# Kernel tuning notes

Measured on AMD Instinct MI355X. Metric: run time of the kernel, lower is better.

The kernel has to match this reference:

```python
import jax, jax.numpy as jnp
import numpy as np

RES = (64, 64)
TEMP = 0.1  # forward default temp

def _mgrid(res):
    # matches torch.meshgrid(linspace(0, r-1, r)...) with default 'ij' indexing
    gs = jnp.meshgrid(*[jnp.arange(r, dtype=jnp.float32) for r in res], indexing='ij')
    return jnp.stack(gs, 0)  # [2, H, W]

def setup_inputs() -> dict:
    key = jax.random.key(0)
    k1, k2 = jax.random.split(key)
    x = jax.random.normal(k1, (8, 32, RES[0], RES[1]), dtype=jnp.float32)
    of = jax.random.normal(k2, (8, 2, RES[0], RES[1]), dtype=jnp.float32)
    return {"x": x, "of": of}

def reference(x, of):
    bs, C = x.shape[0], x.shape[1]
    hw = RES[0] * RES[1]
    gpos = _mgrid(RES).reshape(2, hw)                 # [2, HW] target pixel positions
    opos = gpos[None] + of.reshape(bs, 2, hw)         # [bs, 2, HW] flow-displaced source positions
    # L1 distance: logits[b, i, j] = sum_c |opos[b, c, j] - gpos[c, i]|
    dist = jnp.abs(opos[:, :, None, :] - gpos[None, :, :, None]).sum(axis=1)  # [bs, HW, HW]
    # softmax over target axis i (dim=-2 in torch) -> each source pixel j distributes mass over targets
    locs = jax.nn.softmax(-dist / TEMP, axis=1)       # [bs, HW, HW]
    # out[b, c, i] = sum_j x[b, c, j] * locs[b, i, j]
    out = jnp.einsum('bij,bcj->bci', locs, x.reshape(bs, C, hw))
    return out.reshape(bs, C, RES[0], RES[1])
```

## Files before the change

kernel.cpp:

```cpp
#include <hip/hip_runtime.h>
#include <math.h>

#define HW    4096
#define NC    32
#define NB    8
#define TINV  10.0f
#define RWIN  8
#define WDIM  (8 + 2 * RWIN)
#define RCUT  2.5f


__global__ __launch_bounds__(256) void prep_kernel(
    const float* __restrict__ x, const float* __restrict__ of,
    float4* __restrict__ params, float* __restrict__ xt)
{
    __shared__ float tile[32][257];
    int b  = blockIdx.x >> 4;
    int j0 = (blockIdx.x & 15) << 8;
    int t  = threadIdx.x;
    int j  = j0 + t;

    float oy = (float)(j >> 6) + of[(b * 2 + 0) * HW + j];
    float ox = (float)(j & 63) + of[(b * 2 + 1) * HW + j];

    int cy0 = min(max((int)floorf(oy), 0), 63);
    int cx0 = min(max((int)floorf(ox), 0), 63);
    float Dy = 0.f, Dx = 0.f;
    #pragma unroll
    for (int d = -3; d <= 3; ++d) {
        int iy = cy0 + d, ix = cx0 + d;
        if ((unsigned)iy < 64u) Dy += __expf(-TINV * fabsf(oy - (float)iy));
        if ((unsigned)ix < 64u) Dx += __expf(-TINV * fabsf(ox - (float)ix));
    }
    params[(b << 12) + j] = make_float4(oy, ox, 1.f / Dy, 1.f / Dx);

    #pragma unroll
    for (int c = 0; c < NC; ++c)
        tile[c][t] = x[((b * NC + c) << 12) + j];
    __syncthreads();
    #pragma unroll
    for (int k = 0; k < NC; ++k) {
        int o  = k * 256 + t;
        int jj = o >> 5, c = o & 31;
        xt[((size_t)((b << 12) + j0 + jj)) * NC + c] = tile[c][jj];
    }
}

__global__ __launch_bounds__(256) void gather_kernel(
    const float4* __restrict__ params, const float4* __restrict__ xt4,
    float* __restrict__ out)
{
    __shared__ float  red[4 * 64 * 17];
    __shared__ float4 wp[4][64];
    __shared__ int    sj[4][64];

    const int b    = blockIdx.z;
    const int h    = blockIdx.y;
    const int tile = blockIdx.x;
    const int ty0  = (tile >> 3) << 3;
    const int tx0  = (tile & 7) << 3;

    const int tid  = threadIdx.x;
    const int lane = tid & 63;
    const int wv   = __builtin_amdgcn_readfirstlane(tid >> 6);

    const float iy = (float)(ty0 + (lane >> 3));
    const float ix = (float)(tx0 + (lane & 7));

    float acc[16];
    #pragma unroll
    for (int c = 0; c < 16; ++c) acc[c] = 0.f;

    const float4* pb = params + (b << 12);
    const float4* xb = xt4 + (size_t)(b << 12) * 8 + h * 4;

    const int srow = lane >> 5;
    const int scol = lane & 31;

    for (int r = 0; r < 3; ++r) {
        int ry = wv + srow * 4 + r * 8;
        int jy = ty0 - RWIN + ry;
        int jx = tx0 - RWIN + scol;
        bool valid = ((unsigned)jy < 64u) && ((unsigned)jx < 64u) && (scol < WDIM);
        int j = (jy << 6) + jx;
        float4 p = pb[valid ? j : 0];
        float cy = fminf(fmaxf(p.x, 0.f), 63.f);
        float cx = fminf(fmaxf(p.y, 0.f), 63.f);
        float dyr = fmaxf(fmaxf((float)ty0 - cy, cy - ((float)ty0 + 7.f)), 0.f);
        float dxr = fmaxf(fmaxf((float)tx0 - cx, cx - ((float)tx0 + 7.f)), 0.f);
        bool pred = valid && (dyr + dxr < RCUT);

        unsigned long long m = __ballot(pred);
        int cnt = __popcll(m);
        if (pred) {
            int pos = __builtin_amdgcn_mbcnt_hi((unsigned)(m >> 32),
                      __builtin_amdgcn_mbcnt_lo((unsigned)m, 0u));
            wp[wv][pos] = p;
            sj[wv][pos] = j;
        }

        for (int k = 0; k < cnt; k += 4) {
            int i0 = k;
            int i1 = min(k + 1, cnt - 1);
            int i2 = min(k + 2, cnt - 1);
            int i3 = min(k + 3, cnt - 1);
            float4 p0 = wp[wv][i0], p1 = wp[wv][i1];
            float4 p2 = wp[wv][i2], p3 = wp[wv][i3];
            int j0 = __builtin_amdgcn_readfirstlane(sj[wv][i0]);
            int j1 = __builtin_amdgcn_readfirstlane(sj[wv][i1]);
            int j2 = __builtin_amdgcn_readfirstlane(sj[wv][i2]);
            int j3 = __builtin_amdgcn_readfirstlane(sj[wv][i3]);

            const float4* x0 = xb + j0 * 8;
            const float4* x1 = xb + j1 * 8;
            const float4* x2 = xb + j2 * 8;
            const float4* x3 = xb + j3 * 8;
            float4 A[4], B[4], C[4], D[4];
            #pragma unroll
            for (int u = 0; u < 4; ++u) A[u] = x0[u];
            #pragma unroll
            for (int u = 0; u < 4; ++u) B[u] = x1[u];
            #pragma unroll
            for (int u = 0; u < 4; ++u) C[u] = x2[u];
            #pragma unroll
            for (int u = 0; u < 4; ++u) D[u] = x3[u];

            float g0 = (__expf(-TINV * fabsf(p0.x - iy)) * p0.z)
                     * (__expf(-TINV * fabsf(p0.y - ix)) * p0.w);
            float g1 = (__expf(-TINV * fabsf(p1.x - iy)) * p1.z)
                     * (__expf(-TINV * fabsf(p1.y - ix)) * p1.w);
            float g2 = (__expf(-TINV * fabsf(p2.x - iy)) * p2.z)
                     * (__expf(-TINV * fabsf(p2.y - ix)) * p2.w);
            float g3 = (__expf(-TINV * fabsf(p3.x - iy)) * p3.z)
                     * (__expf(-TINV * fabsf(p3.y - ix)) * p3.w);
            g1 = (k + 1 < cnt) ? g1 : 0.f;
            g2 = (k + 2 < cnt) ? g2 : 0.f;
            g3 = (k + 3 < cnt) ? g3 : 0.f;

            #pragma unroll
            for (int u = 0; u < 4; ++u) {
                acc[4*u+0] = fmaf(g0, A[u].x, acc[4*u+0]);
                acc[4*u+1] = fmaf(g0, A[u].y, acc[4*u+1]);
                acc[4*u+2] = fmaf(g0, A[u].z, acc[4*u+2]);
                acc[4*u+3] = fmaf(g0, A[u].w, acc[4*u+3]);
            }
            #pragma unroll
            for (int u = 0; u < 4; ++u) {
                acc[4*u+0] = fmaf(g1, B[u].x, acc[4*u+0]);
                acc[4*u+1] = fmaf(g1, B[u].y, acc[4*u+1]);
                acc[4*u+2] = fmaf(g1, B[u].z, acc[4*u+2]);
                acc[4*u+3] = fmaf(g1, B[u].w, acc[4*u+3]);
            }
            #pragma unroll
            for (int u = 0; u < 4; ++u) {
                acc[4*u+0] = fmaf(g2, C[u].x, acc[4*u+0]);
                acc[4*u+1] = fmaf(g2, C[u].y, acc[4*u+1]);
                acc[4*u+2] = fmaf(g2, C[u].z, acc[4*u+2]);
                acc[4*u+3] = fmaf(g2, C[u].w, acc[4*u+3]);
            }
            #pragma unroll
            for (int u = 0; u < 4; ++u) {
                acc[4*u+0] = fmaf(g3, D[u].x, acc[4*u+0]);
                acc[4*u+1] = fmaf(g3, D[u].y, acc[4*u+1]);
                acc[4*u+2] = fmaf(g3, D[u].z, acc[4*u+2]);
                acc[4*u+3] = fmaf(g3, D[u].w, acc[4*u+3]);
            }
        }
    }

    float* myred = red + (wv * 64 + lane) * 17;
    #pragma unroll
    for (int c = 0; c < 16; ++c) myred[c] = acc[c];
    __syncthreads();

    int c   = tid >> 4;
    int t16 = tid & 15;
    #pragma unroll
    for (int k = 0; k < 4; ++k) {
        int t = t16 + 16 * k;
        float s = red[(0 * 64 + t) * 17 + c]
                + red[(1 * 64 + t) * 17 + c]
                + red[(2 * 64 + t) * 17 + c]
                + red[(3 * 64 + t) * 17 + c];
        int ch = h * 16 + c;
        out[(((b << 5) + ch) << 12) + (ty0 + (t >> 3)) * 64 + (tx0 + (t & 7))] = s;
    }
}

extern "C" void kernel_launch(void* const* d_in, const int* in_sizes, int n_in,
                              void* d_out, int out_size, void* d_ws, size_t ws_size,
                              hipStream_t stream) {
    const float* x  = (const float*)d_in[0];
    const float* of = (const float*)d_in[1];
    float* out = (float*)d_out;

    float4* params = (float4*)d_ws;
    float*  xt     = (float*)((char*)d_ws + NB * HW * sizeof(float4));

    prep_kernel<<<dim3(NB * 16), dim3(256), 0, stream>>>(x, of, params, xt);
    gather_kernel<<<dim3(64, 2, NB), dim3(256), 0, stream>>>(params, (const float4*)xt, out);
}
```

Baseline: 74.64 us.

## Compact candidate list across rows and software-pipeline gathers with register-held indices

Each wave now runs the candidate selection for all three row passes first, building one compacted list of up to 192 entries in shared memory, then walks it in a single loop. The loop is software-pipelined, so the feature loads for the next pair of candidates are issued before the FMAs for the current pair. Source indices sit in three per-lane registers and are picked out with readlane instead of being read back from shared memory. This removes per-row loop tails and exposes more load latency hiding, at the cost of more registers and a larger shared-memory footprint.

```diff
diff --git a/kernel.cpp b/kernel.cpp
--- a/kernel.cpp
+++ b/kernel.cpp
@@ -6,8 +6,9 @@
 #define NB    8
 #define TINV  10.0f
 #define RWIN  8
-#define WDIM  (8 + 2 * RWIN)
+#define WDIM  24
 #define RCUT  2.5f
+#define LCAP  192
 
 
 __global__ __launch_bounds__(256) void prep_kernel(
@@ -46,13 +47,45 @@
     }
 }
 
+#define FETCH(idx, Xb, Pb) do {                                         \
+    int ic  = min((idx), cm1);                                          \
+    int sel = ic >> 6;                                                  \
+    int jv  = (sel == 0) ? vj0 : ((sel == 1) ? vj1 : vj2);              \
+    int jj  = __builtin_amdgcn_readlane(jv, ic & 63);                   \
+    const float4* xp = xb + jj * 8;                                     \
+    Xb[0] = xp[0]; Xb[1] = xp[1]; Xb[2] = xp[2]; Xb[3] = xp[3];         \
+    Pb = wp[wv][ic];                                                    \
+} while (0)
+
+#define COMPUTE(Xb, Pb, idx) do {                                       \
+    float gy = __expf(-TINV * fabsf(Pb.x - iy)) * Pb.z;                 \
+    float gx = __expf(-TINV * fabsf(Pb.y - ix)) * Pb.w;                 \
+    float g  = ((idx) < cnt) ? gy * gx : 0.f;                           \
+    acc[ 0] = fmaf(g, Xb[0].x, acc[ 0]);                                \
+    acc[ 1] = fmaf(g, Xb[0].y, acc[ 1]);                                \
+    acc[ 2] = fmaf(g, Xb[0].z, acc[ 2]);                                \
+    acc[ 3] = fmaf(g, Xb[0].w, acc[ 3]);                                \
+    acc[ 4] = fmaf(g, Xb[1].x, acc[ 4]);                                \
+    acc[ 5] = fmaf(g, Xb[1].y, acc[ 5]);                                \
+    acc[ 6] = fmaf(g, Xb[1].z, acc[ 6]);                                \
+    acc[ 7] = fmaf(g, Xb[1].w, acc[ 7]);                                \
+    acc[ 8] = fmaf(g, Xb[2].x, acc[ 8]);                                \
+    acc[ 9] = fmaf(g, Xb[2].y, acc[ 9]);                                \
+    acc[10] = fmaf(g, Xb[2].z, acc[10]);                                \
+    acc[11] = fmaf(g, Xb[2].w, acc[11]);                                \
+    acc[12] = fmaf(g, Xb[3].x, acc[12]);                                \
+    acc[13] = fmaf(g, Xb[3].y, acc[13]);                                \
+    acc[14] = fmaf(g, Xb[3].z, acc[14]);                                \
+    acc[15] = fmaf(g, Xb[3].w, acc[15]);                                \
+} while (0)
+
 __global__ __launch_bounds__(256) void gather_kernel(
     const float4* __restrict__ params, const float4* __restrict__ xt4,
     float* __restrict__ out)
 {
     __shared__ float  red[4 * 64 * 17];
-    __shared__ float4 wp[4][64];
-    __shared__ int    sj[4][64];
+    __shared__ float4 wp[4][LCAP];
+    __shared__ int    sj[4][LCAP];
 
     const int b    = blockIdx.z;
     const int h    = blockIdx.y;
@@ -77,6 +110,8 @@
     const int srow = lane >> 5;
     const int scol = lane & 31;
 
+    int cnt = 0;
+    #pragma unroll
     for (int r = 0; r < 3; ++r) {
         int ry = wv + srow * 4 + r * 8;
         int jy = ty0 - RWIN + ry;
@@ -91,80 +126,37 @@
         bool pred = valid && (dyr + dxr < RCUT);
 
         unsigned long long m = __ballot(pred);
-        int cnt = __popcll(m);
         if (pred) {
-            int pos = __builtin_amdgcn_mbcnt_hi((unsigned)(m >> 32),
-                      __builtin_amdgcn_mbcnt_lo((unsigned)m, 0u));
+            int pos = cnt + __builtin_amdgcn_mbcnt_hi((unsigned)(m >> 32),
+                            __builtin_amdgcn_mbcnt_lo((unsigned)m, 0u));
             wp[wv][pos] = p;
             sj[wv][pos] = j;
         }
+        cnt += __popcll(m);
+    }
 
-        for (int k = 0; k < cnt; k += 4) {
-            int i0 = k;
-            int i1 = min(k + 1, cnt - 1);
-            int i2 = min(k + 2, cnt - 1);
-            int i3 = min(k + 3, cnt - 1);
-            float4 p0 = wp[wv][i0], p1 = wp[wv][i1];
-            float4 p2 = wp[wv][i2], p3 = wp[wv][i3];
-            int j0 = __builtin_amdgcn_readfirstlane(sj[wv][i0]);
-            int j1 = __builtin_amdgcn_readfirstlane(sj[wv][i1]);
-            int j2 = __builtin_amdgcn_readfirstlane(sj[wv][i2]);
-            int j3 = __builtin_amdgcn_readfirstlane(sj[wv][i3]);
+    int vj0 = sj[wv][lane];
+    int vj1 = sj[wv][64 + lane];
+    int vj2 = sj[wv][128 + lane];
 
-            const float4* x0 = xb + j0 * 8;
-            const float4* x1 = xb + j1 * 8;
-            const float4* x2 = xb + j2 * 8;
-            const float4* x3 = xb + j3 * 8;
-            float4 A[4], B[4], C[4], D[4];
-            #pragma unroll
-            for (int u = 0; u < 4; ++u) A[u] = x0[u];
-            #pragma unroll
-            for (int u = 0; u < 4; ++u) B[u] = x1[u];
-            #pragma unroll
-            for (int u = 0; u < 4; ++u) C[u] = x2[u];
-            #pragma unroll
-            for (int u = 0; u < 4; ++u) D[u] = x3[u];
-
-            float g0 = (__expf(-TINV * fabsf(p0.x - iy)) * p0.z)
-                     * (__expf(-TINV * fabsf(p0.y - ix)) * p0.w);
-            float g1 = (__expf(-TINV * fabsf(p1.x - iy)) * p1.z)
-                     * (__expf(-TINV * fabsf(p1.y - ix)) * p1.w);
-            float g2 = (__expf(-TINV * fabsf(p2.x - iy)) * p2.z)
-                     * (__expf(-TINV * fabsf(p2.y - ix)) * p2.w);
-            float g3 = (__expf(-TINV * fabsf(p3.x - iy)) * p3.z)
-                     * (__expf(-TINV * fabsf(p3.y - ix)) * p3.w);
-            g1 = (k + 1 < cnt) ? g1 : 0.f;
-            g2 = (k + 2 < cnt) ? g2 : 0.f;
-            g3 = (k + 3 < cnt) ? g3 : 0.f;
-
-            #pragma unroll
-            for (int u = 0; u < 4; ++u) {
-                acc[4*u+0] = fmaf(g0, A[u].x, acc[4*u+0]);
-                acc[4*u+1] = fmaf(g0, A[u].y, acc[4*u+1]);
-                acc[4*u+2] = fmaf(g0, A[u].z, acc[4*u+2]);
-                acc[4*u+3] = fmaf(g0, A[u].w, acc[4*u+3]);
+    if (cnt > 0) {
+        const int cm1  = cnt - 1;
+        const int cnt4 = (cnt + 3) & ~3;
+        float4 X0[4], X1[4], X2[4], X3[4];
+        float4 P0, P1, P2, P3;
+        FETCH(0, X0, P0);
+        FETCH(1, X1, P1);
+        for (int k = 0; k < cnt4; k += 4) {
+            FETCH(k + 2, X2, P2);
+            FETCH(k + 3, X3, P3);
+            COMPUTE(X0, P0, k + 0);
+            COMPUTE(X1, P1, k + 1);
+            if (k + 4 < cnt4) {
+                FETCH(k + 4, X0, P0);
+                FETCH(k + 5, X1, P1);
             }
-            #pragma unroll
-            for (int u = 0; u < 4; ++u) {
-                acc[4*u+0] = fmaf(g1, B[u].x, acc[4*u+0]);
-                acc[4*u+1] = fmaf(g1, B[u].y, acc[4*u+1]);
-                acc[4*u+2] = fmaf(g1, B[u].z, acc[4*u+2]);
-                acc[4*u+3] = fmaf(g1, B[u].w, acc[4*u+3]);
-            }
-            #pragma unroll
-            for (int u = 0; u < 4; ++u) {
-                acc[4*u+0] = fmaf(g2, C[u].x, acc[4*u+0]);
-                acc[4*u+1] = fmaf(g2, C[u].y, acc[4*u+1]);
-                acc[4*u+2] = fmaf(g2, C[u].z, acc[4*u+2]);
-                acc[4*u+3] = fmaf(g2, C[u].w, acc[4*u+3]);
-            }
-            #pragma unroll
-            for (int u = 0; u < 4; ++u) {
-                acc[4*u+0] = fmaf(g3, D[u].x, acc[4*u+0]);
-                acc[4*u+1] = fmaf(g3, D[u].y, acc[4*u+1]);
-                acc[4*u+2] = fmaf(g3, D[u].z, acc[4*u+2]);
-                acc[4*u+3] = fmaf(g3, D[u].w, acc[4*u+3]);
-            }
+            COMPUTE(X2, P2, k + 2);
+            COMPUTE(X3, P3, k + 3);
         }
     }
 
```

After: 79.19 us. 6.1% more time.

## Split gather window rows across four blocks and combine with atomic adds

Applied to the files above, without the earlier changes.

The 24x24 candidate window of each output tile is split by row residue across four blocks, so the grid has four times as many blocks. Each wave now handles at most 36 candidates in a single ballot pass instead of three, and the inner loop is unrolled by two instead of four. Partial sums are merged with atomicAdd into an output that is zeroed by a memset first. The aim is more parallelism and shorter per-block serial loops, at the cost of an extra memset, atomic write traffic and more redundant tile setup.

```diff
diff --git a/kernel.cpp b/kernel.cpp
--- a/kernel.cpp
+++ b/kernel.cpp
@@ -6,8 +6,9 @@
 #define NB    8
 #define TINV  10.0f
 #define RWIN  8
-#define WDIM  (8 + 2 * RWIN)
+#define WDIM  24
 #define RCUT  2.5f
+#define LCAP  40
 
 
 __global__ __launch_bounds__(256) void prep_kernel(
@@ -51,11 +52,12 @@
     float* __restrict__ out)
 {
     __shared__ float  red[4 * 64 * 17];
-    __shared__ float4 wp[4][64];
-    __shared__ int    sj[4][64];
+    __shared__ float4 wp[4][LCAP];
+    __shared__ int    sj[4][LCAP];
 
     const int b    = blockIdx.z;
-    const int h    = blockIdx.y;
+    const int h    = blockIdx.y & 1;
+    const int q    = blockIdx.y >> 1;
     const int tile = blockIdx.x;
     const int ty0  = (tile >> 3) << 3;
     const int tx0  = (tile & 7) << 3;
@@ -74,97 +76,64 @@
     const float4* pb = params + (b << 12);
     const float4* xb = xt4 + (size_t)(b << 12) * 8 + h * 4;
 
-    const int srow = lane >> 5;
-    const int scol = lane & 31;
+    int  ci  = wv + (lane << 2);
+    bool lv  = (lane < 36);
+    int  rr  = ci / 24;
+    int  cc  = ci - rr * 24;
+    int  row = q + (rr << 2);
+    int  jy  = ty0 - RWIN + row;
+    int  jx  = tx0 - RWIN + cc;
+    bool valid = lv && ((unsigned)jy < 64u) && ((unsigned)jx < 64u);
+    int  j   = (jy << 6) + jx;
+    float4 p = pb[valid ? j : 0];
+    float cy = fminf(fmaxf(p.x, 0.f), 63.f);
+    float cx = fminf(fmaxf(p.y, 0.f), 63.f);
+    float dyr = fmaxf(fmaxf((float)ty0 - cy, cy - ((float)ty0 + 7.f)), 0.f);
+    float dxr = fmaxf(fmaxf((float)tx0 - cx, cx - ((float)tx0 + 7.f)), 0.f);
+    bool pred = valid && (dyr + dxr < RCUT);
 
-    for (int r = 0; r < 3; ++r) {
-        int ry = wv + srow * 4 + r * 8;
-        int jy = ty0 - RWIN + ry;
-        int jx = tx0 - RWIN + scol;
-        bool valid = ((unsigned)jy < 64u) && ((unsigned)jx < 64u) && (scol < WDIM);
-        int j = (jy << 6) + jx;
-        float4 p = pb[valid ? j : 0];
-        float cy = fminf(fmaxf(p.x, 0.f), 63.f);
-        float cx = fminf(fmaxf(p.y, 0.f), 63.f);
-        float dyr = fmaxf(fmaxf((float)ty0 - cy, cy - ((float)ty0 + 7.f)), 0.f);
-        float dxr = fmaxf(fmaxf((float)tx0 - cx, cx - ((float)tx0 + 7.f)), 0.f);
-        bool pred = valid && (dyr + dxr < RCUT);
+    unsigned long long m = __ballot(pred);
+    int cnt = __popcll(m);
+    if (pred) {
+        int pos = __builtin_amdgcn_mbcnt_hi((unsigned)(m >> 32),
+                  __builtin_amdgcn_mbcnt_lo((unsigned)m, 0u));
+        wp[wv][pos] = p;
+        sj[wv][pos] = j;
+    }
 
-        unsigned long long m = __ballot(pred);
-        int cnt = __popcll(m);
-        if (pred) {
-            int pos = __builtin_amdgcn_mbcnt_hi((unsigned)(m >> 32),
-                      __builtin_amdgcn_mbcnt_lo((unsigned)m, 0u));
-            wp[wv][pos] = p;
-            sj[wv][pos] = j;
+    for (int k = 0; k < cnt; k += 2) {
+        int i1 = min(k + 1, cnt - 1);
+        float4 p0 = wp[wv][k], p1 = wp[wv][i1];
+        int j0 = __builtin_amdgcn_readfirstlane(sj[wv][k]);
+        int j1 = __builtin_amdgcn_readfirstlane(sj[wv][i1]);
+
+        const float4* x0 = xb + j0 * 8;
+        const float4* x1 = xb + j1 * 8;
+        float4 A[4], B[4];
+        #pragma unroll
+        for (int u = 0; u < 4; ++u) A[u] = x0[u];
+        #pragma unroll
+        for (int u = 0; u < 4; ++u) B[u] = x1[u];
+
+        float g0 = (__expf(-TINV * fabsf(p0.x - iy)) * p0.z)
+                 * (__expf(-TINV * fabsf(p0.y - ix)) * p0.w);
+        float g1 = (__expf(-TINV * fabsf(p1.x - iy)) * p1.z)
+                 * (__expf(-TINV * fabsf(p1.y - ix)) * p1.w);
+        g1 = (k + 1 < cnt) ? g1 : 0.f;
+
+        #pragma unroll
+        for (int u = 0; u < 4; ++u) {
+            acc[4*u+0] = fmaf(g0, A[u].x, acc[4*u+0]);
+            acc[4*u+1] = fmaf(g0, A[u].y, acc[4*u+1]);
+            acc[4*u+2] = fmaf(g0, A[u].z, acc[4*u+2]);
+            acc[4*u+3] = fmaf(g0, A[u].w, acc[4*u+3]);
         }
-
-        for (int k = 0; k < cnt; k += 4) {
-            int i0 = k;
-            int i1 = min(k + 1, cnt - 1);
-            int i2 = min(k + 2, cnt - 1);
-            int i3 = min(k + 3, cnt - 1);
-            float4 p0 = wp[wv][i0], p1 = wp[wv][i1];
-            float4 p2 = wp[wv][i2], p3 = wp[wv][i3];
-            int j0 = __builtin_amdgcn_readfirstlane(sj[wv][i0]);
-            int j1 = __builtin_amdgcn_readfirstlane(sj[wv][i1]);
-            int j2 = __builtin_amdgcn_readfirstlane(sj[wv][i2]);
-            int j3 = __builtin_amdgcn_readfirstlane(sj[wv][i3]);
-
-            const float4* x0 = xb + j0 * 8;
-            const float4* x1 = xb + j1 * 8;
-            const float4* x2 = xb + j2 * 8;
-            const float4* x3 = xb + j3 * 8;
-            float4 A[4], B[4], C[4], D[4];
-            #pragma unroll
-            for (int u = 0; u < 4; ++u) A[u] = x0[u];
-            #pragma unroll
-            for (int u = 0; u < 4; ++u) B[u] = x1[u];
-            #pragma unroll
-            for (int u = 0; u < 4; ++u) C[u] = x2[u];
-            #pragma unroll
-            for (int u = 0; u < 4; ++u) D[u] = x3[u];
-
-            float g0 = (__expf(-TINV * fabsf(p0.x - iy)) * p0.z)
-                     * (__expf(-TINV * fabsf(p0.y - ix)) * p0.w);
-            float g1 = (__expf(-TINV * fabsf(p1.x - iy)) * p1.z)
-                     * (__expf(-TINV * fabsf(p1.y - ix)) * p1.w);
-            float g2 = (__expf(-TINV * fabsf(p2.x - iy)) * p2.z)
-                     * (__expf(-TINV * fabsf(p2.y - ix)) * p2.w);
-            float g3 = (__expf(-TINV * fabsf(p3.x - iy)) * p3.z)
-                     * (__expf(-TINV * fabsf(p3.y - ix)) * p3.w);
-            g1 = (k + 1 < cnt) ? g1 : 0.f;
-            g2 = (k + 2 < cnt) ? g2 : 0.f;
-            g3 = (k + 3 < cnt) ? g3 : 0.f;
-
-            #pragma unroll
-            for (int u = 0; u < 4; ++u) {
-                acc[4*u+0] = fmaf(g0, A[u].x, acc[4*u+0]);
-                acc[4*u+1] = fmaf(g0, A[u].y, acc[4*u+1]);
-                acc[4*u+2] = fmaf(g0, A[u].z, acc[4*u+2]);
-                acc[4*u+3] = fmaf(g0, A[u].w, acc[4*u+3]);
-            }
-            #pragma unroll
-            for (int u = 0; u < 4; ++u) {
-                acc[4*u+0] = fmaf(g1, B[u].x, acc[4*u+0]);
-                acc[4*u+1] = fmaf(g1, B[u].y, acc[4*u+1]);
-                acc[4*u+2] = fmaf(g1, B[u].z, acc[4*u+2]);
-                acc[4*u+3] = fmaf(g1, B[u].w, acc[4*u+3]);
-            }
-            #pragma unroll
-            for (int u = 0; u < 4; ++u) {
-                acc[4*u+0] = fmaf(g2, C[u].x, acc[4*u+0]);
-                acc[4*u+1] = fmaf(g2, C[u].y, acc[4*u+1]);
-                acc[4*u+2] = fmaf(g2, C[u].z, acc[4*u+2]);
-                acc[4*u+3] = fmaf(g2, C[u].w, acc[4*u+3]);
-            }
-            #pragma unroll
-            for (int u = 0; u < 4; ++u) {
-                acc[4*u+0] = fmaf(g3, D[u].x, acc[4*u+0]);
-                acc[4*u+1] = fmaf(g3, D[u].y, acc[4*u+1]);
-                acc[4*u+2] = fmaf(g3, D[u].z, acc[4*u+2]);
-                acc[4*u+3] = fmaf(g3, D[u].w, acc[4*u+3]);
-            }
+        #pragma unroll
+        for (int u = 0; u < 4; ++u) {
+            acc[4*u+0] = fmaf(g1, B[u].x, acc[4*u+0]);
+            acc[4*u+1] = fmaf(g1, B[u].y, acc[4*u+1]);
+            acc[4*u+2] = fmaf(g1, B[u].z, acc[4*u+2]);
+            acc[4*u+3] = fmaf(g1, B[u].w, acc[4*u+3]);
         }
     }
 
@@ -183,7 +152,8 @@
                 + red[(2 * 64 + t) * 17 + c]
                 + red[(3 * 64 + t) * 17 + c];
         int ch = h * 16 + c;
-        out[(((b << 5) + ch) << 12) + (ty0 + (t >> 3)) * 64 + (tx0 + (t & 7))] = s;
+        atomicAdd(&out[(((b << 5) + ch) << 12)
+                       + (ty0 + (t >> 3)) * 64 + (tx0 + (t & 7))], s);
     }
 }
 
@@ -197,6 +167,7 @@
     float4* params = (float4*)d_ws;
     float*  xt     = (float*)((char*)d_ws + NB * HW * sizeof(float4));
 
+    hipMemsetAsync(d_out, 0, (size_t)out_size * sizeof(float), stream);
     prep_kernel<<<dim3(NB * 16), dim3(256), 0, stream>>>(x, of, params, xt);
-    gather_kernel<<<dim3(64, 2, NB), dim3(256), 0, stream>>>(params, (const float4*)xt, out);
+    gather_kernel<<<dim3(64, 8, NB), dim3(256), 0, stream>>>(params, (const float4*)xt, out);
 }
```

Result: slower. 90.96 us (+21.9%).
